# Kernel tuning notes

Measured on AMD Instinct MI355X. Metric: run time of the kernel, lower is better.

Reference implementation:

```python
import jax, jax.numpy as jnp
import numpy as np

DIM = 2048
N_HEADS = 32
HEAD_DIM = DIM // N_HEADS  # 64
ROT_DIM = 32               # partial_rotary_factor = 32/head_dim
ROPE_THETA = 1000000.0
T = 2048
QKV_DIM = 3 * DIM


def setup_inputs() -> dict:
    key = jax.random.key(0)
    ks = jax.random.split(key, 8)
    inp = {
        "positions": jnp.arange(T, dtype=jnp.int32),
        "hidden_states": jax.random.normal(ks[0], (T, DIM), dtype=jnp.float32),
        "Wqkv": jax.random.normal(ks[1], (QKV_DIM, DIM), dtype=jnp.float32) * 0.02,
        "bqkv": jax.random.normal(ks[2], (QKV_DIM,), dtype=jnp.float32) * 0.02,
        "Wout": jax.random.normal(ks[3], (DIM, DIM), dtype=jnp.float32) * 0.02,
        "bout": jax.random.normal(ks[4], (DIM,), dtype=jnp.float32) * 0.02,
        "tau_alpha": jax.random.normal(ks[5], (N_HEADS,), dtype=jnp.float32) * 0.1,
        "tau_wq": jax.random.normal(ks[6], (N_HEADS, QKV_DIM), dtype=jnp.float32) * 0.02,
        "tau_wv": jax.random.normal(ks[7], (N_HEADS, QKV_DIM), dtype=jnp.float32) * 0.02,
    }
    return inp


def _rope_neox(x, positions):
    # x: [T, H, D]; rotate first ROT_DIM dims, neox (half-split) style
    half = ROT_DIM // 2
    inv_freq = 1.0 / (ROPE_THETA ** (jnp.arange(0, ROT_DIM, 2, dtype=jnp.float32) / ROT_DIM))
    ang = positions.astype(jnp.float32)[:, None] * inv_freq[None, :]  # [T, half]
    cos = jnp.cos(ang)[:, None, :]  # [T, 1, half]
    sin = jnp.sin(ang)[:, None, :]
    x1 = x[..., :half]
    x2 = x[..., half:ROT_DIM]
    rot = jnp.concatenate([x1 * cos - x2 * sin, x2 * cos + x1 * sin], axis=-1)
    return jnp.concatenate([rot, x[..., ROT_DIM:]], axis=-1)


def reference(positions, hidden_states, Wqkv, bqkv, Wout, bout, tau_alpha, tau_wq, tau_wv):
    T_, H, D = hidden_states.shape[0], N_HEADS, HEAD_DIM
    qkv = hidden_states @ Wqkv.T + bqkv  # [T, 3*DIM]
    q, k, v = jnp.split(qkv, [DIM, 2 * DIM], axis=-1)

    # tau gating (exact-erf gelu, matching torch F.gelu default)
    tok_feat = jax.nn.gelu(qkv, approximate=False)
    tok_q = jnp.tanh(tok_feat @ tau_wq.T)  # [T, H]
    tok_v = jnp.tanh(tok_feat @ tau_wv.T)
    pos_log = jnp.log(jnp.clip(positions.astype(jnp.float32) + 1.0, 1e-6))  # [T]
    tau_pos = 1.0 + (jax.nn.sigmoid(tau_alpha[None, :] * pos_log[:, None]) - 0.5)  # [T, H]
    tau_q = tok_q + tau_pos
    tau_v = tok_v + tau_pos

    q = q.reshape(T_, H, D) * tau_q[:, :, None]
    k = k.reshape(T_, H, D)
    v = v.reshape(T_, H, D) * tau_v[:, :, None]

    q = _rope_neox(q, positions)
    k = _rope_neox(k, positions)

    # causal attention
    scale = D ** -0.5
    scores = jnp.einsum("thd,shd->hts", q, k) * scale  # [H, T, T]
    causal = positions[:, None] >= positions[None, :]   # [T, T]
    scores = jnp.where(causal[None, :, :], scores, jnp.finfo(scores.dtype).min)
    probs = jax.nn.softmax(scores, axis=-1)
    attn = jnp.einsum("hts,shd->thd", probs, v).reshape(T_, DIM)

    return attn @ Wout.T + bout
```

## Files before the change

kernel.cpp:

```cpp
#include <hip/hip_runtime.h>
#include <math.h>


typedef __bf16 bf16x8 __attribute__((ext_vector_type(8)));
typedef float floatx4 __attribute__((ext_vector_type(4)));
typedef unsigned short ushort8v __attribute__((ext_vector_type(8)));

__device__ __forceinline__ unsigned short f2b(float x) {
    unsigned int b = __float_as_uint(x);
    b = b + 0x7FFFu + ((b >> 16) & 1u);
    return (unsigned short)(b >> 16);
}
__device__ __forceinline__ unsigned short f2b_trunc(float x) {
    return (unsigned short)(__float_as_uint(x) >> 16);
}
__device__ __forceinline__ float b2f(unsigned short u) {
    return __uint_as_float(((unsigned int)u) << 16);
}
__device__ __forceinline__ float gelu_f(float x) {
    return 0.5f * x * (1.0f + erff(x * 0.70710678118654752440f));
}
__device__ __forceinline__ float fexp2(float x) {
    return __builtin_amdgcn_exp2f(x);
}
__device__ __forceinline__ floatx4 mfma16(bf16x8 a, bf16x8 b, floatx4 c) {
    return __builtin_amdgcn_mfma_f32_16x16x32_bf16(a, b, c, 0, 0, 0);
}
__device__ __forceinline__ void gl2lds16(const unsigned short* g, unsigned short* l) {
    __builtin_amdgcn_global_load_lds(
        (__attribute__((address_space(1))) void*)g,
        (__attribute__((address_space(3))) void*)l, 16, 0, 0);
}

__constant__ float INV_FREQ[16] = {
    1.0f, 0.42169650342858224f, 0.17782794100389228f, 0.074989420933245582f,
    0.031622776601683791f, 0.013335214321633240f, 0.0056234132519034908f,
    0.0023713737056616552f, 0.001f, 4.2169650342858224e-4f,
    1.7782794100389228e-4f, 7.4989420933245582e-5f, 3.1622776601683791e-5f,
    1.3335214321633240e-5f, 5.6234132519034908e-6f, 2.3713737056616552e-6f
};

__constant__ unsigned char CHUNK_QT[40] = {
    15,15,15, 14,14,14, 13,13,13, 12,12,12, 11,11, 10,10, 9,9, 8,8, 7,6,5,4,
    15,11,7,3, 14,10,6,2, 13,9,5,1, 12,8,4,0};
__constant__ unsigned char CHUNK_C[40] = {
    0,1,2, 0,1,2, 0,1,2, 0,1,2, 0,1, 0,1, 0,1, 0,1, 0,0,0,0,
    3,2,1,0, 3,2,1,0, 3,2,1,0, 3,2,1,0};

__global__ __launch_bounds__(256) void cvt3_f32_bf16(
    const float* __restrict__ s0, unsigned short* __restrict__ d0, int n0,
    const float* __restrict__ s1, unsigned short* __restrict__ d1, int n1,
    const float* __restrict__ s2, unsigned short* __restrict__ d2, int n2) {
    int i = blockIdx.x * 256 + threadIdx.x;
    const float* s; unsigned short* d;
    if (i < n0)           { s = s0; d = d0; }
    else if (i < n0 + n1) { i -= n0; s = s1; d = d1; }
    else                  { i -= n0 + n1; s = s2; d = d2; if (i >= n2) return; }
    const float4* sp = reinterpret_cast<const float4*>(s) + (size_t)i * 2;
    float4 a = sp[0], b = sp[1];
    ushort8v r;
    r[0] = f2b(a.x); r[1] = f2b(a.y); r[2] = f2b(a.z); r[3] = f2b(a.w);
    r[4] = f2b(b.x); r[5] = f2b(b.y); r[6] = f2b(b.z); r[7] = f2b(b.w);
    *(reinterpret_cast<ushort8v*>(d) + i) = r;
}

__global__ __launch_bounds__(512, 2) void gemm_qkv_8ph(
    const unsigned short* __restrict__ A, const unsigned short* __restrict__ B,
    const float* __restrict__ bias, unsigned short* __restrict__ P,
    int M, int N, int K) {
    __shared__ unsigned short Ls[2][4][8192];
    const int tid = threadIdx.x;
    const int wave = tid >> 6, lane = tid & 63;
    const int row16 = lane & 15, quad = lane >> 4;
    const int wrow = wave >> 2, wcol = wave & 3;
    const int bm0 = blockIdx.y * 256, bn0 = blockIdx.x * 256;
    const int NT = K >> 6;

    floatx4 acc[8][4] = {};

    auto stage_half = [&](int kt, int hf) {
        const unsigned short* mat = (hf & 1) ? B : A;
        const int rbase = (hf & 1) ? bn0 : bm0;
        const int colb = kt * 64 + (hf >> 1) * 32;
        unsigned short* dst = &Ls[kt & 1][hf][0];
        #pragma unroll
        for (int rd = 0; rd < 2; ++rd) {
            int g = tid + rd * 512;
            int rl = g & 7, c4 = (g >> 3) & 3, r8 = g >> 5;
            gl2lds16(mat + (size_t)(rbase + r8 * 8 + rl) * K + colb + c4 * 8,
                     dst + g * 8);
        }
    };

    #pragma unroll
    for (int h = 0; h < 7; ++h) stage_half(h >> 2, h & 3);
    asm volatile("s_waitcnt vmcnt(6)" ::: "memory");
    __builtin_amdgcn_s_barrier();

    const int ra = wrow * 128 + row16;
    const int rb = wcol * 64 + row16;
    const int aoff = (ra >> 3) * 256 + quad * 64 + (ra & 7) * 8;
    const int boff = (rb >> 3) * 256 + quad * 64 + (rb & 7) * 8;

    for (int kt = 0; kt < NT; ++kt) {
        const int bsel = kt & 1;
        bf16x8 af[8], bfr[2];
        #pragma unroll
        for (int mt = 0; mt < 8; ++mt)
            af[mt] = *reinterpret_cast<const bf16x8*>(&Ls[bsel][0][aoff + mt * 512]);
        bfr[0] = *reinterpret_cast<const bf16x8*>(&Ls[bsel][1][boff]);
        bfr[1] = *reinterpret_cast<const bf16x8*>(&Ls[bsel][1][boff + 512]);
        if (kt + 1 < NT) stage_half(kt + 1, 3);
        __builtin_amdgcn_s_barrier();
        asm volatile("s_waitcnt lgkmcnt(0)" ::: "memory");
        __builtin_amdgcn_sched_barrier(0);
        __builtin_amdgcn_s_setprio(1);
        #pragma unroll
        for (int mt = 0; mt < 8; ++mt) {
            acc[mt][0] = mfma16(af[mt], bfr[0], acc[mt][0]);
            acc[mt][1] = mfma16(af[mt], bfr[1], acc[mt][1]);
        }
        __builtin_amdgcn_s_setprio(0);
        __builtin_amdgcn_s_barrier();
        bfr[0] = *reinterpret_cast<const bf16x8*>(&Ls[bsel][1][boff + 1024]);
        bfr[1] = *reinterpret_cast<const bf16x8*>(&Ls[bsel][1][boff + 1536]);
        if (kt + 2 < NT) stage_half(kt + 2, 0);
        __builtin_amdgcn_s_barrier();
        asm volatile("s_waitcnt lgkmcnt(0)" ::: "memory");
        __builtin_amdgcn_sched_barrier(0);
        __builtin_amdgcn_s_setprio(1);
        #pragma unroll
        for (int mt = 0; mt < 8; ++mt) {
            acc[mt][2] = mfma16(af[mt], bfr[0], acc[mt][2]);
            acc[mt][3] = mfma16(af[mt], bfr[1], acc[mt][3]);
        }
        __builtin_amdgcn_s_setprio(0);
        __builtin_amdgcn_s_barrier();
        #pragma unroll
        for (int mt = 0; mt < 8; ++mt)
            af[mt] = *reinterpret_cast<const bf16x8*>(&Ls[bsel][2][aoff + mt * 512]);
        bfr[0] = *reinterpret_cast<const bf16x8*>(&Ls[bsel][3][boff]);
        bfr[1] = *reinterpret_cast<const bf16x8*>(&Ls[bsel][3][boff + 512]);
        if (kt + 2 < NT) stage_half(kt + 2, 1);
        __builtin_amdgcn_s_barrier();
        asm volatile("s_waitcnt lgkmcnt(0)" ::: "memory");
        __builtin_amdgcn_sched_barrier(0);
        __builtin_amdgcn_s_setprio(1);
        #pragma unroll
        for (int mt = 0; mt < 8; ++mt) {
            acc[mt][0] = mfma16(af[mt], bfr[0], acc[mt][0]);
            acc[mt][1] = mfma16(af[mt], bfr[1], acc[mt][1]);
        }
        __builtin_amdgcn_s_setprio(0);
        __builtin_amdgcn_s_barrier();
        bfr[0] = *reinterpret_cast<const bf16x8*>(&Ls[bsel][3][boff + 1024]);
        bfr[1] = *reinterpret_cast<const bf16x8*>(&Ls[bsel][3][boff + 1536]);
        if (kt + 2 < NT) stage_half(kt + 2, 2);
        if (kt == NT - 2)     asm volatile("s_waitcnt vmcnt(0)" ::: "memory");
        else if (kt < NT - 2) asm volatile("s_waitcnt vmcnt(6)" ::: "memory");
        __builtin_amdgcn_s_barrier();
        asm volatile("s_waitcnt lgkmcnt(0)" ::: "memory");
        __builtin_amdgcn_sched_barrier(0);
        __builtin_amdgcn_s_setprio(1);
        #pragma unroll
        for (int mt = 0; mt < 8; ++mt) {
            acc[mt][2] = mfma16(af[mt], bfr[0], acc[mt][2]);
            acc[mt][3] = mfma16(af[mt], bfr[1], acc[mt][3]);
        }
        __builtin_amdgcn_s_setprio(0);
        __builtin_amdgcn_s_barrier();
    }

    #pragma unroll
    for (int mt = 0; mt < 8; ++mt) {
        #pragma unroll
        for (int nt = 0; nt < 4; ++nt) {
            int gc = bn0 + wcol * 64 + nt * 16 + row16;
            float bv = bias[gc];
            int gr0 = bm0 + wrow * 128 + mt * 16 + quad * 4;
            #pragma unroll
            for (int i = 0; i < 4; ++i)
                P[(size_t)(gr0 + i) * N + gc] = f2b(acc[mt][nt][i] + bv);
        }
    }
}

template <int BM, int BN, bool OUT_BF16>
__global__ __launch_bounds__(256) void gemm_bf16_bt(
    const unsigned short* __restrict__ A, const unsigned short* __restrict__ B,
    const float* __restrict__ bias, void* __restrict__ Cout,
    int M, int N, int K) {
    constexpr int MT = BM / 32, NT = BN / 32;
    __shared__ unsigned short As[BM * 64];
    __shared__ unsigned short Bs[BN * 64];
    const int tid = threadIdx.x;
    const int wave = tid >> 6, lane = tid & 63;
    const int row16 = lane & 15, quad = lane >> 4;
    const int wm = (wave >> 1) * (BM / 2), wn = (wave & 1) * (BN / 2);
    const int bm0 = blockIdx.y * BM, bn0 = blockIdx.x * BN;
    const int rl = lane & 7, cl = lane >> 3;

    floatx4 acc[MT][NT] = {};

    for (int k0 = 0; k0 < K; k0 += 64) {
        __syncthreads();
        #pragma unroll
        for (int j = 0; j < BM / 32; ++j) {
            int unit = wave * (BM / 32) + j;
            const unsigned short* ga = A + (size_t)(bm0 + unit * 8 + rl) * K + k0 + cl * 8;
            gl2lds16(ga, &As[unit * 512 + lane * 8]);
        }
        #pragma unroll
        for (int j = 0; j < BN / 32; ++j) {
            int unit = wave * (BN / 32) + j;
            const unsigned short* gb = B + (size_t)(bn0 + unit * 8 + rl) * K + k0 + cl * 8;
            gl2lds16(gb, &Bs[unit * 512 + lane * 8]);
        }
        __syncthreads();

        #pragma unroll
        for (int ks = 0; ks < 2; ++ks) {
            bf16x8 af[MT], bfr[NT];
            #pragma unroll
            for (int mt = 0; mt < MT; ++mt) {
                int r = wm + mt * 16 + row16;
                af[mt] = *reinterpret_cast<const bf16x8*>(
                    &As[(r >> 3) * 512 + (ks * 4 + quad) * 64 + (r & 7) * 8]);
            }
            #pragma unroll
            for (int nt = 0; nt < NT; ++nt) {
                int r = wn + nt * 16 + row16;
                bfr[nt] = *reinterpret_cast<const bf16x8*>(
                    &Bs[(r >> 3) * 512 + (ks * 4 + quad) * 64 + (r & 7) * 8]);
            }
            #pragma unroll
            for (int mt = 0; mt < MT; ++mt)
                #pragma unroll
                for (int nt = 0; nt < NT; ++nt)
                    acc[mt][nt] = mfma16(af[mt], bfr[nt], acc[mt][nt]);
        }
    }

    #pragma unroll
    for (int mt = 0; mt < MT; ++mt) {
        #pragma unroll
        for (int nt = 0; nt < NT; ++nt) {
            int gc = bn0 + wn + nt * 16 + row16;
            float bv = bias[gc];
            int gr0 = bm0 + wm + mt * 16 + quad * 4;
            #pragma unroll
            for (int i = 0; i < 4; ++i) {
                float v = acc[mt][nt][i] + bv;
                if (OUT_BF16)
                    ((unsigned short*)Cout)[(size_t)(gr0 + i) * N + gc] = f2b(v);
                else
                    ((float*)Cout)[(size_t)(gr0 + i) * N + gc] = v;
            }
        }
    }
}

template <int KSPLIT>
__global__ __launch_bounds__(256) void tok_gemm_splitk(
    const unsigned short* __restrict__ A0,
    const float* __restrict__ Bq, const float* __restrict__ Bv,
    float* __restrict__ C, int K) {
    constexpr int LDT = 72;
    __shared__ unsigned short As[64 * LDT];
    __shared__ unsigned short Bs[64 * LDT];
    const int tid = threadIdx.x;
    const int wave = tid >> 6, lane = tid & 63;
    const int row16 = lane & 15, quad = lane >> 4;
    const int wm = (wave >> 1) * 32, wn = (wave & 1) * 32;
    const int bm0 = blockIdx.y * 64;
    const int kbeg = blockIdx.x * KSPLIT;

    floatx4 acc[2][2] = {};

    for (int k0 = kbeg; k0 < kbeg + KSPLIT; k0 += 64) {
        #pragma unroll
        for (int it = 0; it < 2; ++it) {
            int i = tid + it * 256;
            int r = i >> 3, c8 = i & 7;
            size_t off = (size_t)(bm0 + r) * K + k0 + c8 * 8;
            ushort8v a0 = *reinterpret_cast<const ushort8v*>(A0 + off);
            ushort8v g;
            #pragma unroll
            for (int j = 0; j < 8; ++j) g[j] = f2b(gelu_f(b2f(a0[j])));
            *reinterpret_cast<ushort8v*>(&As[r * LDT + c8 * 8]) = g;

            const float* brow = (r < 32) ? (Bq + (size_t)r * K) : (Bv + (size_t)(r - 32) * K);
            float4 w0 = *reinterpret_cast<const float4*>(brow + k0 + c8 * 8);
            float4 w1 = *reinterpret_cast<const float4*>(brow + k0 + c8 * 8 + 4);
            ushort8v wb;
            wb[0] = f2b(w0.x); wb[1] = f2b(w0.y); wb[2] = f2b(w0.z); wb[3] = f2b(w0.w);
            wb[4] = f2b(w1.x); wb[5] = f2b(w1.y); wb[6] = f2b(w1.z); wb[7] = f2b(w1.w);
            *reinterpret_cast<ushort8v*>(&Bs[r * LDT + c8 * 8]) = wb;
        }
        __syncthreads();

        #pragma unroll
        for (int ks = 0; ks < 2; ++ks) {
            bf16x8 af[2], bfr[2];
            #pragma unroll
            for (int mt = 0; mt < 2; ++mt)
                af[mt] = *reinterpret_cast<const bf16x8*>(
                    &As[(wm + mt * 16 + row16) * LDT + ks * 32 + quad * 8]);
            #pragma unroll
            for (int nt = 0; nt < 2; ++nt)
                bfr[nt] = *reinterpret_cast<const bf16x8*>(
                    &Bs[(wn + nt * 16 + row16) * LDT + ks * 32 + quad * 8]);
            #pragma unroll
            for (int mt = 0; mt < 2; ++mt)
                #pragma unroll
                for (int nt = 0; nt < 2; ++nt)
                    acc[mt][nt] = mfma16(af[mt], bfr[nt], acc[mt][nt]);
        }
        __syncthreads();
    }

    #pragma unroll
    for (int mt = 0; mt < 2; ++mt)
        #pragma unroll
        for (int nt = 0; nt < 2; ++nt) {
            int gc = wn + nt * 16 + row16;
            int gr0 = bm0 + wm + mt * 16 + quad * 4;
            #pragma unroll
            for (int i = 0; i < 4; ++i)
                atomicAdd(&C[(size_t)(gr0 + i) * 64 + gc], acc[mt][nt][i]);
        }
}

__global__ __launch_bounds__(256) void qkv_process(
    const unsigned short* __restrict__ P,
    const float* __restrict__ tok_raw, const float* __restrict__ tau_alpha,
    const int* __restrict__ positions, unsigned short* __restrict__ qh,
    unsigned short* __restrict__ kh, unsigned short* __restrict__ vpk) {
    const int h = blockIdx.y;
    const int t0 = blockIdx.x * 64;
    const int tid = threadIdx.x;
    __shared__ float vtr[64][65];
    __shared__ float tauq_s[64], tauv_s[64];

    if (tid < 64) {
        int t = t0 + tid;
        float pos = (float)positions[t];
        float pl = logf(fmaxf(pos + 1.0f, 1e-6f));
        float a = tau_alpha[h];
        float tp = 0.5f + 1.0f / (1.0f + __expf(-a * pl));
        tauq_s[tid] = tanhf(tok_raw[t * 64 + h]) + tp;
        tauv_s[tid] = tanhf(tok_raw[t * 64 + 32 + h]) + tp;
    }
    __syncthreads();

    const float QSCALE = 0.18033688011112042f;
    #pragma unroll
    for (int it = 0; it < 2; ++it) {
        int idx = tid + it * 256;
        int tl = idx >> 3, c8 = idx & 7;
        int t = t0 + tl;
        size_t rb = (size_t)t * 6144 + h * 64 + c8 * 8;
        ushort8v q0v = *reinterpret_cast<const ushort8v*>(P + rb);
        ushort8v k0v = *reinterpret_cast<const ushort8v*>(P + rb + 2048);
        ushort8v v0v = *reinterpret_cast<const ushort8v*>(P + rb + 4096);
        float tq = tauq_s[tl], tv = tauv_s[tl];
        float qo[8], ko[8];
        #pragma unroll
        for (int j = 0; j < 8; ++j) {
            qo[j] = b2f(q0v[j]) * tq;
            ko[j] = b2f(k0v[j]);
        }
        if (c8 < 4) {
            size_t rp = (size_t)t * 6144 + h * 64 + (c8 ^ 2) * 8;
            ushort8v qp0 = *reinterpret_cast<const ushort8v*>(P + rp);
            ushort8v kp0 = *reinterpret_cast<const ushort8v*>(P + rp + 2048);
            float pos = (float)positions[t];
            float sgn = (c8 < 2) ? -1.0f : 1.0f;
            #pragma unroll
            for (int j = 0; j < 8; ++j) {
                int fi = (c8 * 8 + j) & 15;
                float ang = pos * INV_FREQ[fi];
                float s, c;
                sincosf(ang, &s, &c);
                float qp = b2f(qp0[j]) * tq;
                float kp = b2f(kp0[j]);
                qo[j] = qo[j] * c + sgn * qp * s;
                ko[j] = ko[j] * c + sgn * kp * s;
            }
        }
        size_t ob = ((size_t)h * 2048 + t) * 64 + c8 * 8;
        ushort8v qw, kw;
        #pragma unroll
        for (int j = 0; j < 8; ++j) {
            qw[j] = f2b(qo[j] * QSCALE);
            kw[j] = f2b(ko[j]);
        }
        *reinterpret_cast<ushort8v*>(qh + ob) = qw;
        *reinterpret_cast<ushort8v*>(kh + ob) = kw;
        #pragma unroll
        for (int j = 0; j < 8; ++j)
            vtr[c8 * 8 + j][tl] = b2f(v0v[j]) * tv;
    }
    __syncthreads();
    #pragma unroll
    for (int it = 0; it < 2; ++it) {
        int idx = tid + it * 256;
        int d = idx >> 3, tc = (idx & 7) * 8;
        int sb = (t0 + tc) >> 5;
        int quad = (tc & 31) >> 3;
        int nt = d >> 4, m = d & 15;
        ushort8v w;
        #pragma unroll
        for (int j = 0; j < 8; ++j) w[j] = f2b(vtr[d][tc + j]);
        *reinterpret_cast<ushort8v*>(
            vpk + (size_t)h * 131072 + sb * 2048 + nt * 512 + quad * 128 + m * 8) = w;
    }
}

__global__ __launch_bounds__(256) void attn_fa(
    const unsigned short* __restrict__ qh, const unsigned short* __restrict__ kh,
    const unsigned short* __restrict__ vpk, unsigned short* __restrict__ Opart,
    float* __restrict__ ml) {
    constexpr int LD = 72;
    __shared__ unsigned short pbuf[4][2][16 * LD];
    const int b = blockIdx.x;
    const int h = (b & 7) + 8 * ((b >> 3) & 3);
    const int cpos = b >> 5;
    const int qt = CHUNK_QT[cpos], ch = CHUNK_C[cpos];
    const int q0 = qt * 128;
    const int slot = (h * 16 + qt) * 4 + ch;
    const int wave = threadIdx.x >> 6, lane = threadIdx.x & 63;
    const int m = lane & 15, quad = lane >> 4;
    const int qrow0 = q0 + wave * 32;
    const int sbeg = ch * 512;
    const int send = min(sbeg + 512, qrow0 + 32);

    bf16x8 aq[2][2];
    #pragma unroll
    for (int mt = 0; mt < 2; ++mt) {
        const unsigned short* qptr = qh + ((size_t)h * 2048 + qrow0 + mt * 16 + m) * 64;
        aq[mt][0] = *reinterpret_cast<const bf16x8*>(qptr + quad * 8);
        aq[mt][1] = *reinterpret_cast<const bf16x8*>(qptr + 32 + quad * 8);
    }
    const unsigned short* kbase = kh + (size_t)h * 2048 * 64;
    const unsigned short* vbase = vpk + (size_t)h * 131072;

    floatx4 o[2][4] = {};
    float lsum[2][4] = {};

    for (int s0 = sbeg; s0 < send; s0 += 64) {
        floatx4 sc[2][4];
        #pragma unroll
        for (int sg = 0; sg < 4; ++sg) {
            const unsigned short* kr = kbase + (size_t)(s0 + sg * 16 + m) * 64;
            bf16x8 bk0 = *reinterpret_cast<const bf16x8*>(kr + quad * 8);
            bf16x8 bk1 = *reinterpret_cast<const bf16x8*>(kr + 32 + quad * 8);
            #pragma unroll
            for (int mt = 0; mt < 2; ++mt) {
                floatx4 z = {};
                z = mfma16(aq[mt][0], bk0, z);
                z = mfma16(aq[mt][1], bk1, z);
                sc[mt][sg] = z;
            }
        }
        if (s0 + 63 > qrow0) {
            #pragma unroll
            for (int mt = 0; mt < 2; ++mt)
                #pragma unroll
                for (int sg = 0; sg < 4; ++sg)
                    #pragma unroll
                    for (int i = 0; i < 4; ++i) {
                        int t = qrow0 + mt * 16 + quad * 4 + i;
                        int s = s0 + sg * 16 + m;
                        sc[mt][sg][i] = (s > t) ? -1e30f : sc[mt][sg][i];
                    }
        }
        #pragma unroll
        for (int mt = 0; mt < 2; ++mt)
            #pragma unroll
            for (int sg = 0; sg < 4; ++sg)
                #pragma unroll
                for (int i = 0; i < 4; ++i)
                    sc[mt][sg][i] = fexp2(sc[mt][sg][i]);
        #pragma unroll
        for (int mt = 0; mt < 2; ++mt)
            #pragma unroll
            for (int i = 0; i < 4; ++i)
                lsum[mt][i] += (sc[mt][0][i] + sc[mt][1][i]) + (sc[mt][2][i] + sc[mt][3][i]);

        unsigned short* pb0 = pbuf[wave][0];
        unsigned short* pb1 = pbuf[wave][1];
        #pragma unroll
        for (int sg = 0; sg < 4; ++sg)
            #pragma unroll
            for (int i = 0; i < 4; ++i) {
                pb0[(quad * 4 + i) * LD + sg * 16 + m] = f2b_trunc(sc[0][sg][i]);
                pb1[(quad * 4 + i) * LD + sg * 16 + m] = f2b_trunc(sc[1][sg][i]);
            }
        bf16x8 ap[2][2];
        #pragma unroll
        for (int mt = 0; mt < 2; ++mt) {
            ap[mt][0] = *reinterpret_cast<const bf16x8*>(&pbuf[wave][mt][m * LD + quad * 8]);
            ap[mt][1] = *reinterpret_cast<const bf16x8*>(&pbuf[wave][mt][m * LD + 32 + quad * 8]);
        }
        #pragma unroll
        for (int c = 0; c < 2; ++c) {
            const unsigned short* vrow = vbase + ((s0 >> 5) + c) * 2048;
            #pragma unroll
            for (int nt = 0; nt < 4; ++nt) {
                bf16x8 bv = *reinterpret_cast<const bf16x8*>(vrow + nt * 512 + lane * 8);
                o[0][nt] = mfma16(ap[0][c], bv, o[0][nt]);
                o[1][nt] = mfma16(ap[1][c], bv, o[1][nt]);
            }
        }
    }

    #pragma unroll
    for (int d = 1; d < 16; d <<= 1)
        #pragma unroll
        for (int mt = 0; mt < 2; ++mt)
            #pragma unroll
            for (int i = 0; i < 4; ++i)
                lsum[mt][i] += __shfl_xor(lsum[mt][i], d, 16);
    #pragma unroll
    for (int mt = 0; mt < 2; ++mt) {
        #pragma unroll
        for (int nt = 0; nt < 4; ++nt)
            #pragma unroll
            for (int i = 0; i < 4; ++i)
                Opart[((size_t)slot * 128 + wave * 32 + mt * 16 + quad * 4 + i) * 64 + nt * 16 + m]
                    = f2b(o[mt][nt][i]);
        if (m == 0) {
            #pragma unroll
            for (int i = 0; i < 4; ++i)
                ml[(size_t)slot * 128 + wave * 32 + mt * 16 + quad * 4 + i] = lsum[mt][i];
        }
    }
}

__global__ __launch_bounds__(256) void attn_merge(
    const unsigned short* __restrict__ Opart, const float* __restrict__ ml,
    unsigned short* __restrict__ attnb) {
    const int qt = blockIdx.x, h = blockIdx.y;
    const int nc = qt / 4 + 1;
    const int tid = threadIdx.x;
    const int r = tid >> 1, dh = (tid & 1) * 32;
    const int bs = (h * 16 + qt) * 4;

    float denom = 0.0f;
    #pragma unroll
    for (int c = 0; c < 4; ++c)
        if (c < nc) denom += ml[(size_t)(bs + c) * 128 + r];
    float inv = 1.0f / denom;

    float acc[32] = {};
    #pragma unroll
    for (int c = 0; c < 4; ++c) {
        if (c < nc) {
            const unsigned short* op = Opart + ((size_t)(bs + c) * 128 + r) * 64 + dh;
            #pragma unroll
            for (int j = 0; j < 4; ++j) {
                ushort8v v = *reinterpret_cast<const ushort8v*>(op + j * 8);
                #pragma unroll
                for (int k = 0; k < 8; ++k)
                    acc[j * 8 + k] += b2f(v[k]);
            }
        }
    }
    unsigned short* dst = attnb + (size_t)(qt * 128 + r) * 2048 + h * 64 + dh;
    #pragma unroll
    for (int j = 0; j < 4; ++j) {
        ushort8v v;
        #pragma unroll
        for (int k = 0; k < 8; ++k) v[k] = f2b(acc[j * 8 + k] * inv);
        *reinterpret_cast<ushort8v*>(dst + j * 8) = v;
    }
}

extern "C" void kernel_launch(void* const* d_in, const int* in_sizes, int n_in,
                              void* d_out, int out_size, void* d_ws, size_t ws_size,
                              hipStream_t stream) {
    const int*   positions = (const int*)d_in[0];
    const float* hidden    = (const float*)d_in[1];
    const float* Wqkv      = (const float*)d_in[2];
    const float* bqkv      = (const float*)d_in[3];
    const float* Wout      = (const float*)d_in[4];
    const float* bout      = (const float*)d_in[5];
    const float* tau_alpha = (const float*)d_in[6];
    const float* tau_wq    = (const float*)d_in[7];
    const float* tau_wv    = (const float*)d_in[8];

    unsigned char* ws = (unsigned char*)d_ws;
    unsigned short* P       = (unsigned short*)(ws);
    unsigned short* Opart   = (unsigned short*)(ws);
    unsigned short* wqb     = (unsigned short*)(ws + 50331648);
    unsigned short* qh      = (unsigned short*)(ws + 50331648);
    unsigned short* kh      = (unsigned short*)(ws + 58720256);
    unsigned short* vpk     = (unsigned short*)(ws + 67108864);
    unsigned short* hb      = (unsigned short*)(ws + 75497472);
    float*          tok_raw = (float*)(ws + 75497472);
    unsigned short* attnb   = (unsigned short*)(ws + 75497472);
    float*          ml      = (float*)(ws + 83886080);
    unsigned short* wob     = (unsigned short*)(ws + 85983232);

    cvt3_f32_bf16<<<10240, 256, 0, stream>>>(
        hidden, hb, 524288, Wqkv, wqb, 1572864, Wout, wob, 524288);
    gemm_qkv_8ph<<<dim3(24, 8), 512, 0, stream>>>(
        hb, wqb, bqkv, P, 2048, 6144, 2048);
    hipMemsetAsync(tok_raw, 0, (size_t)2048 * 64 * 4, stream);
    tok_gemm_splitk<256><<<dim3(24, 32), 256, 0, stream>>>(
        P, tau_wq, tau_wv, tok_raw, 6144);
    qkv_process<<<dim3(32, 32), 256, 0, stream>>>(
        P, tok_raw, tau_alpha, positions, qh, kh, vpk);
    attn_fa<<<1280, 256, 0, stream>>>(qh, kh, vpk, Opart, ml);
    attn_merge<<<dim3(16, 32), 256, 0, stream>>>(Opart, ml, attnb);
    gemm_bf16_bt<128, 128, false><<<dim3(16, 16), 256, 0, stream>>>(
        attnb, wob, bout, d_out, 2048, 2048, 2048);
}
```

Measured before the change: 368.9 us.

## Ping-pong register prefetch in QKV GEMM and smaller tiles for output GEMM

Restructures the 8-phase QKV GEMM main loop so LDS fragments for the next quadrant are loaded into ping/pong register sets while the current quadrant's MFMAs run, and moves global staging to after each barrier. The intent is to hide LDS read latency behind matrix work and cut barriers per k-step. Separately, the output projection GEMM switches from 128x128 to 64x64 tiles, launching 1024 blocks instead of 256 for better CU occupancy. The cost is more registers for the fragment buffers and less data reuse per block in the output GEMM.

```diff
diff --git a/kernel.cpp b/kernel.cpp
--- a/kernel.cpp
+++ b/kernel.cpp
@@ -102,73 +102,86 @@
     const int aoff = (ra >> 3) * 256 + quad * 64 + (ra & 7) * 8;
     const int boff = (rb >> 3) * 256 + quad * 64 + (rb & 7) * 8;
 
+    bf16x8 Aping[4], Apong[4], Bping[4], Bpong[4];
+    #pragma unroll
+    for (int i = 0; i < 4; ++i) {
+        Aping[i] = *reinterpret_cast<const bf16x8*>(&Ls[0][0][aoff + i * 512]);
+        Bping[i] = *reinterpret_cast<const bf16x8*>(&Ls[0][1][boff + i * 512]);
+    }
+
     for (int kt = 0; kt < NT; ++kt) {
         const int bsel = kt & 1;
-        bf16x8 af[8], bfr[2];
-        #pragma unroll
-        for (int mt = 0; mt < 8; ++mt)
-            af[mt] = *reinterpret_cast<const bf16x8*>(&Ls[bsel][0][aoff + mt * 512]);
-        bfr[0] = *reinterpret_cast<const bf16x8*>(&Ls[bsel][1][boff]);
-        bfr[1] = *reinterpret_cast<const bf16x8*>(&Ls[bsel][1][boff + 512]);
-        if (kt + 1 < NT) stage_half(kt + 1, 3);
-        __builtin_amdgcn_s_barrier();
         asm volatile("s_waitcnt lgkmcnt(0)" ::: "memory");
         __builtin_amdgcn_sched_barrier(0);
+        #pragma unroll
+        for (int i = 0; i < 4; ++i)
+            Apong[i] = *reinterpret_cast<const bf16x8*>(&Ls[bsel][0][aoff + (4 + i) * 512]);
+        __builtin_amdgcn_sched_barrier(0);
         __builtin_amdgcn_s_setprio(1);
         #pragma unroll
-        for (int mt = 0; mt < 8; ++mt) {
-            acc[mt][0] = mfma16(af[mt], bfr[0], acc[mt][0]);
-            acc[mt][1] = mfma16(af[mt], bfr[1], acc[mt][1]);
-        }
+        for (int mt = 0; mt < 4; ++mt)
+            #pragma unroll
+            for (int nt = 0; nt < 4; ++nt)
+                acc[mt][nt] = mfma16(Aping[mt], Bping[nt], acc[mt][nt]);
         __builtin_amdgcn_s_setprio(0);
         __builtin_amdgcn_s_barrier();
-        bfr[0] = *reinterpret_cast<const bf16x8*>(&Ls[bsel][1][boff + 1024]);
-        bfr[1] = *reinterpret_cast<const bf16x8*>(&Ls[bsel][1][boff + 1536]);
-        if (kt + 2 < NT) stage_half(kt + 2, 0);
-        __builtin_amdgcn_s_barrier();
+        if (kt + 1 < NT) stage_half(kt + 1, 3);
         asm volatile("s_waitcnt lgkmcnt(0)" ::: "memory");
         __builtin_amdgcn_sched_barrier(0);
+        #pragma unroll
+        for (int i = 0; i < 4; ++i) {
+            Aping[i] = *reinterpret_cast<const bf16x8*>(&Ls[bsel][2][aoff + i * 512]);
+            Bpong[i] = *reinterpret_cast<const bf16x8*>(&Ls[bsel][3][boff + i * 512]);
+        }
+        __builtin_amdgcn_sched_barrier(0);
         __builtin_amdgcn_s_setprio(1);
         #pragma unroll
-        for (int mt = 0; mt < 8; ++mt) {
-            acc[mt][2] = mfma16(af[mt], bfr[0], acc[mt][2]);
-            acc[mt][3] = mfma16(af[mt], bfr[1], acc[mt][3]);
-        }
+        for (int mt = 0; mt < 4; ++mt)
+            #pragma unroll
+            for (int nt = 0; nt < 4; ++nt)
+                acc[4 + mt][nt] = mfma16(Apong[mt], Bping[nt], acc[4 + mt][nt]);
         __builtin_amdgcn_s_setprio(0);
         __builtin_amdgcn_s_barrier();
-        #pragma unroll
-        for (int mt = 0; mt < 8; ++mt)
-            af[mt] = *reinterpret_cast<const bf16x8*>(&Ls[bsel][2][aoff + mt * 512]);
-        bfr[0] = *reinterpret_cast<const bf16x8*>(&Ls[bsel][3][boff]);
-        bfr[1] = *reinterpret_cast<const bf16x8*>(&Ls[bsel][3][boff + 512]);
-        if (kt + 2 < NT) stage_half(kt + 2, 1);
-        __builtin_amdgcn_s_barrier();
+        if (kt + 2 < NT) stage_half(kt + 2, 0);
         asm volatile("s_waitcnt lgkmcnt(0)" ::: "memory");
         __builtin_amdgcn_sched_barrier(0);
+        #pragma unroll
+        for (int i = 0; i < 4; ++i)
+            Apong[i] = *reinterpret_cast<const bf16x8*>(&Ls[bsel][2][aoff + (4 + i) * 512]);
+        __builtin_amdgcn_sched_barrier(0);
         __builtin_amdgcn_s_setprio(1);
         #pragma unroll
-        for (int mt = 0; mt < 8; ++mt) {
-            acc[mt][0] = mfma16(af[mt], bfr[0], acc[mt][0]);
-            acc[mt][1] = mfma16(af[mt], bfr[1], acc[mt][1]);
-        }
+        for (int mt = 0; mt < 4; ++mt)
+            #pragma unroll
+            for (int nt = 0; nt < 4; ++nt)
+                acc[mt][nt] = mfma16(Aping[mt], Bpong[nt], acc[mt][nt]);
         __builtin_amdgcn_s_setprio(0);
         __builtin_amdgcn_s_barrier();
-        bfr[0] = *reinterpret_cast<const bf16x8*>(&Ls[bsel][3][boff + 1024]);
-        bfr[1] = *reinterpret_cast<const bf16x8*>(&Ls[bsel][3][boff + 1536]);
-        if (kt + 2 < NT) stage_half(kt + 2, 2);
-        if (kt == NT - 2)     asm volatile("s_waitcnt vmcnt(0)" ::: "memory");
-        else if (kt < NT - 2) asm volatile("s_waitcnt vmcnt(6)" ::: "memory");
-        __builtin_amdgcn_s_barrier();
+        if (kt + 2 < NT) stage_half(kt + 2, 1);
+        if (kt <= NT - 2) {
+            if (kt == NT - 2) asm volatile("s_waitcnt vmcnt(0)" ::: "memory");
+            else              asm volatile("s_waitcnt vmcnt(4)" ::: "memory");
+            __builtin_amdgcn_s_barrier();
+        }
         asm volatile("s_waitcnt lgkmcnt(0)" ::: "memory");
         __builtin_amdgcn_sched_barrier(0);
+        if (kt + 1 < NT) {
+            #pragma unroll
+            for (int i = 0; i < 4; ++i) {
+                Aping[i] = *reinterpret_cast<const bf16x8*>(&Ls[bsel ^ 1][0][aoff + i * 512]);
+                Bping[i] = *reinterpret_cast<const bf16x8*>(&Ls[bsel ^ 1][1][boff + i * 512]);
+            }
+        }
+        __builtin_amdgcn_sched_barrier(0);
         __builtin_amdgcn_s_setprio(1);
         #pragma unroll
-        for (int mt = 0; mt < 8; ++mt) {
-            acc[mt][2] = mfma16(af[mt], bfr[0], acc[mt][2]);
-            acc[mt][3] = mfma16(af[mt], bfr[1], acc[mt][3]);
-        }
+        for (int mt = 0; mt < 4; ++mt)
+            #pragma unroll
+            for (int nt = 0; nt < 4; ++nt)
+                acc[4 + mt][nt] = mfma16(Apong[mt], Bpong[nt], acc[4 + mt][nt]);
         __builtin_amdgcn_s_setprio(0);
         __builtin_amdgcn_s_barrier();
+        if (kt + 2 < NT) stage_half(kt + 2, 2);
     }
 
     #pragma unroll
@@ -614,6 +627,6 @@
         P, tok_raw, tau_alpha, positions, qh, kh, vpk);
     attn_fa<<<1280, 256, 0, stream>>>(qh, kh, vpk, Opart, ml);
     attn_merge<<<dim3(16, 32), 256, 0, stream>>>(Opart, ml, attnb);
-    gemm_bf16_bt<128, 128, false><<<dim3(16, 16), 256, 0, stream>>>(
+    gemm_bf16_bt<64, 64, false><<<dim3(32, 32), 256, 0, stream>>>(
         attnb, wob, bout, d_out, 2048, 2048, 2048);
 }
```

Result: slower. 376.5 us (+2.1%).
